# Optimization experiments

Hardware: AMD Instinct MI355X
Metric: run time of the kernel (lower is better)

The kernel has to match this reference:

```python
import jax, jax.numpy as jnp
import numpy as np

DIM = 1024
H = 16
D = DIM // H
B = 4
N = 1024
SUPPRESS = 0.1
SCALE = D ** -0.5


def setup_inputs() -> dict:
    key = jax.random.key(0)
    ks = jax.random.split(key, 16)
    s = 0.02
    inp = {
        "x": jax.random.normal(ks[0], (B, N, DIM), jnp.float32),
        "padding_mask": jax.random.randint(ks[1], (B, N), 0, 2).astype(bool),
        "alibi_bias": jax.random.normal(ks[2], (1, H, N, N), jnp.float32),
        "Wq": jax.random.normal(ks[3], (DIM, DIM), jnp.float32) * s,
        "bq": jnp.zeros((DIM,), jnp.float32),
        "Wk": jax.random.normal(ks[4], (DIM, DIM), jnp.float32) * s,
        "bk": jnp.zeros((DIM,), jnp.float32),
        "Wv": jax.random.normal(ks[5], (DIM, DIM), jnp.float32) * s,
        "bv": jnp.zeros((DIM,), jnp.float32),
        "WqC": jax.random.normal(ks[6], (D, D), jnp.float32) * s,
        "WAC": jax.random.normal(ks[7], (D, D), jnp.float32) * s,
        "bC": jax.random.normal(ks[8], (D,), jnp.float32) * s,
        "Wqg": jax.random.normal(ks[9], (D, D), jnp.float32) * s,
        "WAg": jax.random.normal(ks[10], (D, D), jnp.float32) * s,
        "bg": jax.random.normal(ks[11], (D,), jnp.float32) * s,
        "Wo": jax.random.normal(ks[12], (DIM, DIM), jnp.float32) * s,
        "bo": jnp.zeros((DIM,), jnp.float32),
    }
    return inp


def reference(x, padding_mask, alibi_bias, Wq, bq, Wk, bk, Wv, bv,
              WqC, WAC, bC, Wqg, WAg, bg, Wo, bo):
    Bx, Nx, C = x.shape
    # QKV projections -> [B, H, N, D]
    q = (x @ Wq.T + bq).reshape(Bx, Nx, H, D).transpose(0, 2, 1, 3)
    k = (x @ Wk.T + bk).reshape(Bx, Nx, H, D).transpose(0, 2, 1, 3)
    v = (x @ Wv.T + bv).reshape(Bx, Nx, H, D).transpose(0, 2, 1, 3)
    # scores [B, H, N, N] with alibi then key padding mask
    scores = jnp.einsum("bhnd,bhmd->bhnm", q * SCALE, k)
    scores = scores + alibi_bias  # alibi covers all H heads, broadcasts over B
    scores = jnp.where(padding_mask[:, None, None, :], -jnp.inf, scores)
    attn = jax.nn.softmax(scores.astype(jnp.float32), axis=-1).astype(q.dtype)
    A = jnp.einsum("bhnm,bhmd->bhnd", attn, v)
    # per-head gated linear fusion (W_* are D x D, shared across heads)
    C2 = jnp.einsum("bhnd,ed->bhne", q, WqC) + jnp.einsum("bhnd,ed->bhne", A, WAC) + bC
    g = jax.nn.sigmoid(jnp.einsum("bhnd,ed->bhne", q, Wqg) + jnp.einsum("bhnd,ed->bhne", A, WAg) + bg)
    G = (jnp.exp(g) + 1.0) * SUPPRESS
    Aega = G * C2  # [B, H, N, D]
    out = Aega.transpose(0, 2, 1, 3).reshape(Bx, Nx, C)
    return out @ Wo.T + bo
```

## Files before the change

### kernel.cpp

```cpp
#include <hip/hip_runtime.h>
#include <stdint.h>
#include <stddef.h>

#define SEQ   1024
#define CD    1024
#define NHD   16
#define HDD   64
#define NBB   4

typedef unsigned short u16t;
typedef __attribute__((ext_vector_type(4))) float f32x4;
typedef __attribute__((ext_vector_type(4))) unsigned int u32x4;
typedef __attribute__((ext_vector_type(8))) _Float16 f16x8;
typedef __attribute__((ext_vector_type(4))) unsigned short u16x4;

__device__ __forceinline__ u16t f2h(float f) {
  _Float16 h = (_Float16)f;
  return __builtin_bit_cast(u16t, h);
}

__device__ __forceinline__ f32x4 MFMA(u32x4 a, u32x4 b, f32x4 c) {
  return __builtin_amdgcn_mfma_f32_16x16x32_f16(
      __builtin_bit_cast(f16x8, a), __builtin_bit_cast(f16x8, b), c, 0, 0, 0);
}

struct ConvArgs {
  const float* src[9];
  u16t* dst[9];
  int n[9];
};

__global__ void conv_kernel(ConvArgs a) {
  const int tid = blockIdx.x * blockDim.x + threadIdx.x;
  const int nth = gridDim.x * blockDim.x;
  for (int s = 0; s < 9; ++s) {
    const float4* src = (const float4*)a.src[s];
    u16x4* dst = (u16x4*)a.dst[s];
    const int n4 = a.n[s] >> 2;
    for (int i = tid; i < n4; i += nth) {
      float4 f = src[i];
      u16x4 o = { f2h(f.x), f2h(f.y), f2h(f.z), f2h(f.w) };
      dst[i] = o;
    }
  }
}

__global__ void mask_prep_kernel(const void* __restrict__ mask,
                                 float* __restrict__ maskbias) {
  __shared__ int notI32, notU8;
  if (threadIdx.x == 0) { notI32 = 0; notU8 = 0; }
  __syncthreads();
  const unsigned int* mi = (const unsigned int*)mask;
  const unsigned char* mb = (const unsigned char*)mask;
  int nI = 0, nU = 0;
  for (int i = threadIdx.x; i < 1024; i += 256) {
    if (mi[i] > 1u) nI = 1;
  }
  for (int i = threadIdx.x; i < 4096; i += 256) {
    if (mb[i] > 1) nU = 1;
  }
  if (nI) atomicOr(&notI32, 1);
  if (nU) atomicOr(&notU8, 1);
  __syncthreads();
  const int mode = (!notI32) ? 0 : ((!notU8) ? 1 : 2);
  for (int i = threadIdx.x; i < NBB * SEQ; i += 256) {
    bool m;
    if (mode == 0)      m = mi[i] != 0u;
    else if (mode == 1) m = mb[i] != 0;
    else                m = ((const float*)mask)[i] != 0.0f;
    maskbias[i] = m ? -1e30f : 0.0f;
  }
}

template <int MODE>
__global__ __launch_bounds__(256, 2) void gemm_kernel(
    const u16t* __restrict__ A,
    const u16t* __restrict__ B0, const u16t* __restrict__ B1,
    const u16t* __restrict__ B2,
    const float* __restrict__ bias0, const float* __restrict__ bias1,
    const float* __restrict__ bias2,
    void* __restrict__ out0, void* __restrict__ out1, void* __restrict__ out2) {
  __shared__ alignas(16) u16t As[128][40];
  __shared__ alignas(16) u16t Bs[128][40];

  const int tid = threadIdx.x;
  const int m0 = blockIdx.x * 128;
  int n0, mat = 0;
  const u16t* Bsel;
  const float* biassel;
  if constexpr (MODE == 0) {
    mat = (int)blockIdx.y >> 3;
    n0 = ((int)blockIdx.y & 7) * 128;
    Bsel = (mat == 0) ? B0 : ((mat == 1) ? B1 : B2);
    biassel = (mat == 0) ? bias0 : ((mat == 1) ? bias1 : bias2);
  } else {
    n0 = (int)blockIdx.y * 128;
    Bsel = B0;
    biassel = bias0;
  }

  const int sr = tid >> 1;
  const int sc = (tid & 1) * 16;
  const int wid = tid >> 6, lane = tid & 63;
  const int l16 = lane & 15, lq = lane >> 4;
  const int wr = (wid >> 1) * 64, wc = (wid & 1) * 64;

  f32x4 acc[4][4] = {};

  const u16t* Aptr = A + (size_t)(m0 + sr) * CD + sc;
  const u16t* Bptr = Bsel + (size_t)(n0 + sr) * CD + sc;

  for (int k0 = 0; k0 < CD; k0 += 32) {
    u32x4 av0 = *(const u32x4*)(Aptr + k0);
    u32x4 av1 = *(const u32x4*)(Aptr + k0 + 8);
    u32x4 bv0 = *(const u32x4*)(Bptr + k0);
    u32x4 bv1 = *(const u32x4*)(Bptr + k0 + 8);
    __syncthreads();
    *(u32x4*)(&As[sr][sc]) = av0;
    *(u32x4*)(&As[sr][sc + 8]) = av1;
    *(u32x4*)(&Bs[sr][sc]) = bv0;
    *(u32x4*)(&Bs[sr][sc + 8]) = bv1;
    __syncthreads();
    u32x4 af[4], bf[4];
#pragma unroll
    for (int i = 0; i < 4; ++i) {
      af[i] = *(const u32x4*)(&As[wr + i * 16 + l16][lq * 8]);
      bf[i] = *(const u32x4*)(&Bs[wc + i * 16 + l16][lq * 8]);
    }
#pragma unroll
    for (int i = 0; i < 4; ++i)
#pragma unroll
      for (int j = 0; j < 4; ++j)
        acc[i][j] = MFMA(af[i], bf[j], acc[i][j]);
  }

  if constexpr (MODE == 1) {
    float* outp = (float*)out0;
#pragma unroll
    for (int i = 0; i < 4; ++i) {
#pragma unroll
      for (int j = 0; j < 4; ++j) {
        const int col = n0 + wc + j * 16 + l16;
        const float bb = biassel[col];
#pragma unroll
        for (int r = 0; r < 4; ++r) {
          const int row = m0 + wr + i * 16 + lq * 4 + r;
          outp[(size_t)row * CD + col] = acc[i][j][r] + bb;
        }
      }
    }
  } else {
    u16t* outp = (mat == 0) ? (u16t*)out0 : ((mat == 1) ? (u16t*)out1 : (u16t*)out2);
#pragma unroll
    for (int i = 0; i < 4; ++i) {
#pragma unroll
      for (int j = 0; j < 4; ++j) {
        const int cl = n0 + wc + j * 16 + l16;
        const int hh = cl >> 6, dd = cl & 63;
        const float bb = biassel[cl];
#pragma unroll
        for (int r = 0; r < 4; ++r) {
          const int row = m0 + wr + i * 16 + lq * 4 + r;
          const int bidx = row >> 10, nidx = row & 1023;
          outp[(((size_t)(bidx * NHD + hh)) * SEQ + nidx) * HDD + dd] =
              f2h(acc[i][j][r] + bb);
        }
      }
    }
  }
}

__global__ __launch_bounds__(256, 2) void attn_kernel(
    const u16t* __restrict__ Q, const u16t* __restrict__ K,
    const u16t* __restrict__ V, const float* __restrict__ alibi,
    const float* __restrict__ maskbias, u16t* __restrict__ Aout) {
  __shared__ alignas(16) u16t Ks[64][72];
  __shared__ alignas(16) u16t Vt[64][72];
  __shared__ alignas(16) u16t Ps[4][16][72];

  const int qt = blockIdx.x, h = blockIdx.y, b = blockIdx.z;
  const int tid = threadIdx.x, wid = tid >> 6, lane = tid & 63;
  const int l16 = lane & 15, lq = lane >> 4;
  const size_t hoff = ((size_t)(b * NHD + h)) * SEQ * HDD;
  const float* al = alibi + (size_t)h * SEQ * SEQ;
  const float* mb = maskbias + b * SEQ;
  const int q0 = qt * 64 + wid * 16;

  const u32x4 qf0 = *(const u32x4*)(Q + hoff + (size_t)(q0 + l16) * HDD + lq * 8);
  const u32x4 qf1 = *(const u32x4*)(Q + hoff + (size_t)(q0 + l16) * HDD + 32 + lq * 8);

  f32x4 Oacc[4] = {};
  float mrow[4] = {-1e30f, -1e30f, -1e30f, -1e30f};
  float lrow[4] = {0.f, 0.f, 0.f, 0.f};

  const int sr = tid >> 2;
  const int sc = (tid & 3) * 16;

  for (int k0 = 0; k0 < SEQ; k0 += 64) {
    u32x4 kv0 = *(const u32x4*)(K + hoff + (size_t)(k0 + sr) * HDD + sc);
    u32x4 kv1 = *(const u32x4*)(K + hoff + (size_t)(k0 + sr) * HDD + sc + 8);
    u32x4 vv0 = *(const u32x4*)(V + hoff + (size_t)(k0 + sr) * HDD + sc);
    u32x4 vv1 = *(const u32x4*)(V + hoff + (size_t)(k0 + sr) * HDD + sc + 8);
    __syncthreads();
    *(u32x4*)(&Ks[sr][sc]) = kv0;
    *(u32x4*)(&Ks[sr][sc + 8]) = kv1;
    {
      const u16t* pv = (const u16t*)&vv0;
#pragma unroll
      for (int e = 0; e < 8; ++e) Vt[sc + e][sr] = pv[e];
      pv = (const u16t*)&vv1;
#pragma unroll
      for (int e = 0; e < 8; ++e) Vt[sc + 8 + e][sr] = pv[e];
    }
    __syncthreads();

    f32x4 s[4];
#pragma unroll
    for (int kt = 0; kt < 4; ++kt) {
      u32x4 kf0 = *(const u32x4*)(&Ks[kt * 16 + l16][lq * 8]);
      u32x4 kf1 = *(const u32x4*)(&Ks[kt * 16 + l16][32 + lq * 8]);
      f32x4 z = {};
      z = MFMA(qf0, kf0, z);
      z = MFMA(qf1, kf1, z);
      s[kt] = z;
    }
#pragma unroll
    for (int kt = 0; kt < 4; ++kt) {
      const int kc = k0 + kt * 16 + l16;
      const float mbv = mb[kc];
#pragma unroll
      for (int r = 0; r < 4; ++r) {
        const int qr = q0 + lq * 4 + r;
        s[kt][r] = s[kt][r] * 0.125f + al[(size_t)qr * SEQ + kc] + mbv;
      }
    }
    float corr[4];
#pragma unroll
    for (int r = 0; r < 4; ++r) {
      float mx = fmaxf(fmaxf(s[0][r], s[1][r]), fmaxf(s[2][r], s[3][r]));
#pragma unroll
      for (int off = 1; off < 16; off <<= 1)
        mx = fmaxf(mx, __shfl_xor(mx, off, 64));
      const float mnew = fmaxf(mrow[r], mx);
      corr[r] = __expf(mrow[r] - mnew);
      mrow[r] = mnew;
      float ps = 0.f;
#pragma unroll
      for (int kt = 0; kt < 4; ++kt) {
        const float p = __expf(s[kt][r] - mnew);
        s[kt][r] = p;
        ps += p;
      }
#pragma unroll
      for (int off = 1; off < 16; off <<= 1)
        ps += __shfl_xor(ps, off, 64);
      lrow[r] = lrow[r] * corr[r] + ps;
    }
#pragma unroll
    for (int dt = 0; dt < 4; ++dt)
#pragma unroll
      for (int r = 0; r < 4; ++r)
        Oacc[dt][r] *= corr[r];

#pragma unroll
    for (int kt = 0; kt < 4; ++kt)
#pragma unroll
      for (int r = 0; r < 4; ++r)
        Ps[wid][lq * 4 + r][kt * 16 + l16] = f2h(s[kt][r]);

    const u32x4 pf0 = *(const u32x4*)(&Ps[wid][l16][lq * 8]);
    const u32x4 pf1 = *(const u32x4*)(&Ps[wid][l16][32 + lq * 8]);
#pragma unroll
    for (int dt = 0; dt < 4; ++dt) {
      u32x4 vf0 = *(const u32x4*)(&Vt[dt * 16 + l16][lq * 8]);
      u32x4 vf1 = *(const u32x4*)(&Vt[dt * 16 + l16][32 + lq * 8]);
      Oacc[dt] = MFMA(pf0, vf0, Oacc[dt]);
      Oacc[dt] = MFMA(pf1, vf1, Oacc[dt]);
    }
  }

#pragma unroll
  for (int r = 0; r < 4; ++r) {
    const float inv = 1.0f / lrow[r];
    const int qr = q0 + lq * 4 + r;
#pragma unroll
    for (int dt = 0; dt < 4; ++dt)
      Aout[hoff + (size_t)qr * HDD + dt * 16 + l16] = f2h(Oacc[dt][r] * inv);
  }
}

__global__ __launch_bounds__(256, 2) void fuse_kernel(
    const u16t* __restrict__ Q, const u16t* __restrict__ Aatt,
    const u16t* __restrict__ W4, const float* __restrict__ bC,
    const float* __restrict__ bg, u16t* __restrict__ Aega) {
  __shared__ alignas(16) u16t Ws[4][64][72];
  const int tid = threadIdx.x;
  for (int i = tid; i < 2048; i += 256) {
    const int w = i >> 9;
    const int r = (i >> 3) & 63;
    const int c = (i & 7) * 8;
    *(u32x4*)(&Ws[w][r][c]) = *(const u32x4*)(W4 + (size_t)(w * 64 + r) * 64 + c);
  }
  __syncthreads();
  const int wid = tid >> 6, lane = tid & 63;
  const int l16 = lane & 15, lq = lane >> 4;
  const size_t row0 = (size_t)blockIdx.x * 64 + wid * 16;

  const u32x4 qf0 = *(const u32x4*)(Q + (row0 + l16) * HDD + lq * 8);
  const u32x4 qf1 = *(const u32x4*)(Q + (row0 + l16) * HDD + 32 + lq * 8);
  const u32x4 af0 = *(const u32x4*)(Aatt + (row0 + l16) * HDD + lq * 8);
  const u32x4 af1 = *(const u32x4*)(Aatt + (row0 + l16) * HDD + 32 + lq * 8);

#pragma unroll
  for (int et = 0; et < 4; ++et) {
    u32x4 wc0 = *(const u32x4*)(&Ws[0][et * 16 + l16][lq * 8]);
    u32x4 wc1 = *(const u32x4*)(&Ws[0][et * 16 + l16][32 + lq * 8]);
    u32x4 wa0 = *(const u32x4*)(&Ws[1][et * 16 + l16][lq * 8]);
    u32x4 wa1 = *(const u32x4*)(&Ws[1][et * 16 + l16][32 + lq * 8]);
    u32x4 wg0 = *(const u32x4*)(&Ws[2][et * 16 + l16][lq * 8]);
    u32x4 wg1 = *(const u32x4*)(&Ws[2][et * 16 + l16][32 + lq * 8]);
    u32x4 wh0 = *(const u32x4*)(&Ws[3][et * 16 + l16][lq * 8]);
    u32x4 wh1 = *(const u32x4*)(&Ws[3][et * 16 + l16][32 + lq * 8]);
    f32x4 c2 = {};
    c2 = MFMA(qf0, wc0, c2);
    c2 = MFMA(qf1, wc1, c2);
    c2 = MFMA(af0, wa0, c2);
    c2 = MFMA(af1, wa1, c2);
    f32x4 gg = {};
    gg = MFMA(qf0, wg0, gg);
    gg = MFMA(qf1, wg1, gg);
    gg = MFMA(af0, wh0, gg);
    gg = MFMA(af1, wh1, gg);
    const int e = et * 16 + l16;
    const float bCe = bC[e], bge = bg[e];
#pragma unroll
    for (int r = 0; r < 4; ++r) {
      const size_t row = row0 + lq * 4 + r;
      const int bidx = (int)(row >> 14);
      const int hh = (int)((row >> 10) & 15);
      const int nn = (int)(row & 1023);
      const float C2v = c2[r] + bCe;
      const float gv = 1.f / (1.f + __expf(-(gg[r] + bge)));
      const float Gv = (__expf(gv) + 1.f) * 0.1f;
      Aega[((size_t)(bidx * SEQ + nn)) * CD + hh * 64 + e] = f2h(Gv * C2v);
    }
  }
}

static constexpr size_t OFF_X16 = 0;
static constexpr size_t OFF_WQ  = 8388608;
static constexpr size_t OFF_WK  = 10485760;
static constexpr size_t OFF_WV  = 12582912;
static constexpr size_t OFF_WO  = 14680064;
static constexpr size_t OFF_W4  = 16777216;
static constexpr size_t OFF_MB  = 16809984;
static constexpr size_t OFF_Q   = 16826368;
static constexpr size_t OFF_K   = 25214976;
static constexpr size_t OFF_V   = 33603584;
static constexpr size_t OFF_A   = 41992192;
static constexpr size_t OFF_AEG = 50380800;

extern "C" void kernel_launch(void* const* d_in, const int* in_sizes, int n_in,
                              void* d_out, int out_size, void* d_ws, size_t ws_size,
                              hipStream_t stream) {
  const float* x     = (const float*)d_in[0];
  const void*  pmask = d_in[1];
  const float* alibi = (const float*)d_in[2];
  const float* Wq    = (const float*)d_in[3];
  const float* bq    = (const float*)d_in[4];
  const float* Wk    = (const float*)d_in[5];
  const float* bk    = (const float*)d_in[6];
  const float* Wv    = (const float*)d_in[7];
  const float* bv    = (const float*)d_in[8];
  const float* WqC   = (const float*)d_in[9];
  const float* WAC   = (const float*)d_in[10];
  const float* bC    = (const float*)d_in[11];
  const float* Wqg   = (const float*)d_in[12];
  const float* WAg   = (const float*)d_in[13];
  const float* bg    = (const float*)d_in[14];
  const float* Wo    = (const float*)d_in[15];
  const float* bo    = (const float*)d_in[16];

  char* w = (char*)d_ws;
  u16t* X16 = (u16t*)(w + OFF_X16);
  u16t* WQp = (u16t*)(w + OFF_WQ);
  u16t* WKp = (u16t*)(w + OFF_WK);
  u16t* WVp = (u16t*)(w + OFF_WV);
  u16t* WOp = (u16t*)(w + OFF_WO);
  u16t* W4p = (u16t*)(w + OFF_W4);
  float* MBp = (float*)(w + OFF_MB);
  u16t* Qb  = (u16t*)(w + OFF_Q);
  u16t* Kb  = (u16t*)(w + OFF_K);
  u16t* Vb  = (u16t*)(w + OFF_V);
  u16t* Ab  = (u16t*)(w + OFF_A);
  u16t* AEG = (u16t*)(w + OFF_AEG);

  ConvArgs ca;
  ca.src[0] = x;   ca.dst[0] = X16;            ca.n[0] = 4 * 1024 * 1024;
  ca.src[1] = Wq;  ca.dst[1] = WQp;            ca.n[1] = 1024 * 1024;
  ca.src[2] = Wk;  ca.dst[2] = WKp;            ca.n[2] = 1024 * 1024;
  ca.src[3] = Wv;  ca.dst[3] = WVp;            ca.n[3] = 1024 * 1024;
  ca.src[4] = Wo;  ca.dst[4] = WOp;            ca.n[4] = 1024 * 1024;
  ca.src[5] = WqC; ca.dst[5] = W4p;            ca.n[5] = 4096;
  ca.src[6] = WAC; ca.dst[6] = W4p + 4096;     ca.n[6] = 4096;
  ca.src[7] = Wqg; ca.dst[7] = W4p + 8192;     ca.n[7] = 4096;
  ca.src[8] = WAg; ca.dst[8] = W4p + 12288;    ca.n[8] = 4096;

  hipLaunchKernelGGL(conv_kernel, dim3(1024), dim3(256), 0, stream, ca);
  hipLaunchKernelGGL(mask_prep_kernel, dim3(1), dim3(256), 0, stream, pmask, MBp);
  hipLaunchKernelGGL(HIP_KERNEL_NAME(gemm_kernel<0>), dim3(32, 24), dim3(256), 0,
                     stream, X16, WQp, WKp, WVp, bq, bk, bv,
                     (void*)Qb, (void*)Kb, (void*)Vb);
  hipLaunchKernelGGL(attn_kernel, dim3(16, 16, 4), dim3(256), 0, stream,
                     Qb, Kb, Vb, alibi, MBp, Ab);
  hipLaunchKernelGGL(fuse_kernel, dim3(1024), dim3(256), 0, stream,
                     Qb, Ab, W4p, bC, bg, AEG);
  hipLaunchKernelGGL(HIP_KERNEL_NAME(gemm_kernel<1>), dim3(32, 8), dim3(256), 0,
                     stream, AEG, WOp, (const u16t*)nullptr, (const u16t*)nullptr,
                     bo, (const float*)nullptr, (const float*)nullptr,
                     d_out, (void*)nullptr, (void*)nullptr);
}
```

Baseline: 162.5 us.

## Use direct global-to-LDS loads in GEMM, pre-transposed V and pipelined attention

The GEMM now stages A/B tiles with global_load_lds instead of register round-trips and drops the padded LDS layout. The QKV GEMM writes V already transposed, so attention no longer scatters V into LDS element by element. Attention computes S transposed, so each lane holds one query row and softmax needs fewer shuffles. P is passed to the PV MFMA through register shuffles instead of LDS, and K/V/alibi loads are software-prefetched one tile ahead with occupancy raised to 3. Losing the LDS padding may introduce bank conflicts, and the strided transposed V store is less coalesced.

```diff
diff --git a/kernel.cpp b/kernel.cpp
--- a/kernel.cpp
+++ b/kernel.cpp
@@ -22,6 +22,12 @@
 __device__ __forceinline__ f32x4 MFMA(u32x4 a, u32x4 b, f32x4 c) {
   return __builtin_amdgcn_mfma_f32_16x16x32_f16(
       __builtin_bit_cast(f16x8, a), __builtin_bit_cast(f16x8, b), c, 0, 0, 0);
+}
+
+__device__ __forceinline__ void gl_lds16(const u16t* g, u16t* l) {
+  __builtin_amdgcn_global_load_lds(
+      (const __attribute__((address_space(1))) unsigned int*)g,
+      (__attribute__((address_space(3))) unsigned int*)l, 16, 0, 0);
 }
 
 struct ConvArgs {
@@ -80,8 +86,8 @@
     const float* __restrict__ bias0, const float* __restrict__ bias1,
     const float* __restrict__ bias2,
     void* __restrict__ out0, void* __restrict__ out1, void* __restrict__ out2) {
-  __shared__ alignas(16) u16t As[128][40];
-  __shared__ alignas(16) u16t Bs[128][40];
+  __shared__ alignas(16) u16t As[128 * 32];
+  __shared__ alignas(16) u16t Bs[128 * 32];
 
   const int tid = threadIdx.x;
   const int m0 = blockIdx.x * 128;
@@ -99,33 +105,31 @@
     biassel = bias0;
   }
 
-  const int sr = tid >> 1;
-  const int sc = (tid & 1) * 16;
   const int wid = tid >> 6, lane = tid & 63;
   const int l16 = lane & 15, lq = lane >> 4;
   const int wr = (wid >> 1) * 64, wc = (wid & 1) * 64;
 
+  const int srow = lane >> 2;
+  const int scol = (lane & 3) * 8;
+  const u16t* Ag = A + (size_t)(m0 + wid * 32 + srow) * CD + scol;
+  const u16t* Bg = Bsel + (size_t)(n0 + wid * 32 + srow) * CD + scol;
+  u16t* AsW = &As[(wid * 32 + srow) * 32 + scol];
+  u16t* BsW = &Bs[(wid * 32 + srow) * 32 + scol];
+
   f32x4 acc[4][4] = {};
 
-  const u16t* Aptr = A + (size_t)(m0 + sr) * CD + sc;
-  const u16t* Bptr = Bsel + (size_t)(n0 + sr) * CD + sc;
-
   for (int k0 = 0; k0 < CD; k0 += 32) {
-    u32x4 av0 = *(const u32x4*)(Aptr + k0);
-    u32x4 av1 = *(const u32x4*)(Aptr + k0 + 8);
-    u32x4 bv0 = *(const u32x4*)(Bptr + k0);
-    u32x4 bv1 = *(const u32x4*)(Bptr + k0 + 8);
     __syncthreads();
-    *(u32x4*)(&As[sr][sc]) = av0;
-    *(u32x4*)(&As[sr][sc + 8]) = av1;
-    *(u32x4*)(&Bs[sr][sc]) = bv0;
-    *(u32x4*)(&Bs[sr][sc + 8]) = bv1;
+    gl_lds16(Ag + k0, AsW);
+    gl_lds16(Ag + k0 + (size_t)16 * CD, AsW + 16 * 32);
+    gl_lds16(Bg + k0, BsW);
+    gl_lds16(Bg + k0 + (size_t)16 * CD, BsW + 16 * 32);
     __syncthreads();
     u32x4 af[4], bf[4];
 #pragma unroll
     for (int i = 0; i < 4; ++i) {
-      af[i] = *(const u32x4*)(&As[wr + i * 16 + l16][lq * 8]);
-      bf[i] = *(const u32x4*)(&Bs[wc + i * 16 + l16][lq * 8]);
+      af[i] = *(const u32x4*)(&As[(wr + i * 16 + l16) * 32 + lq * 8]);
+      bf[i] = *(const u32x4*)(&Bs[(wc + i * 16 + l16) * 32 + lq * 8]);
     }
 #pragma unroll
     for (int i = 0; i < 4; ++i)
@@ -162,57 +166,82 @@
         for (int r = 0; r < 4; ++r) {
           const int row = m0 + wr + i * 16 + lq * 4 + r;
           const int bidx = row >> 10, nidx = row & 1023;
-          outp[(((size_t)(bidx * NHD + hh)) * SEQ + nidx) * HDD + dd] =
-              f2h(acc[i][j][r] + bb);
+          if (mat == 2) {
+            outp[(((size_t)(bidx * NHD + hh)) * HDD + dd) * SEQ + nidx] =
+                f2h(acc[i][j][r] + bb);
+          } else {
+            outp[(((size_t)(bidx * NHD + hh)) * SEQ + nidx) * HDD + dd] =
+                f2h(acc[i][j][r] + bb);
+          }
         }
       }
     }
   }
 }
 
-__global__ __launch_bounds__(256, 2) void attn_kernel(
+__global__ __launch_bounds__(256, 3) void attn_kernel(
     const u16t* __restrict__ Q, const u16t* __restrict__ K,
-    const u16t* __restrict__ V, const float* __restrict__ alibi,
+    const u16t* __restrict__ VT, const float* __restrict__ alibi,
     const float* __restrict__ maskbias, u16t* __restrict__ Aout) {
   __shared__ alignas(16) u16t Ks[64][72];
-  __shared__ alignas(16) u16t Vt[64][72];
-  __shared__ alignas(16) u16t Ps[4][16][72];
+  __shared__ alignas(16) u16t Vts[64][72];
 
   const int qt = blockIdx.x, h = blockIdx.y, b = blockIdx.z;
   const int tid = threadIdx.x, wid = tid >> 6, lane = tid & 63;
   const int l16 = lane & 15, lq = lane >> 4;
   const size_t hoff = ((size_t)(b * NHD + h)) * SEQ * HDD;
-  const float* al = alibi + (size_t)h * SEQ * SEQ;
+  const int q0 = qt * 64 + wid * 16;
+  const float* al = alibi + (size_t)h * SEQ * SEQ + (size_t)(q0 + l16) * SEQ;
   const float* mb = maskbias + b * SEQ;
-  const int q0 = qt * 64 + wid * 16;
 
   const u32x4 qf0 = *(const u32x4*)(Q + hoff + (size_t)(q0 + l16) * HDD + lq * 8);
   const u32x4 qf1 = *(const u32x4*)(Q + hoff + (size_t)(q0 + l16) * HDD + 32 + lq * 8);
 
   f32x4 Oacc[4] = {};
-  float mrow[4] = {-1e30f, -1e30f, -1e30f, -1e30f};
-  float lrow[4] = {0.f, 0.f, 0.f, 0.f};
+  float mrow = -1e30f, lrow = 0.f;
 
   const int sr = tid >> 2;
   const int sc = (tid & 3) * 16;
-
-  for (int k0 = 0; k0 < SEQ; k0 += 64) {
-    u32x4 kv0 = *(const u32x4*)(K + hoff + (size_t)(k0 + sr) * HDD + sc);
-    u32x4 kv1 = *(const u32x4*)(K + hoff + (size_t)(k0 + sr) * HDD + sc + 8);
-    u32x4 vv0 = *(const u32x4*)(V + hoff + (size_t)(k0 + sr) * HDD + sc);
-    u32x4 vv1 = *(const u32x4*)(V + hoff + (size_t)(k0 + sr) * HDD + sc + 8);
-    __syncthreads();
+  const u16t* Kg = K + hoff + (size_t)sr * HDD + sc;
+  const u16t* Vg = VT + hoff + (size_t)sr * SEQ + sc;
+
+  u32x4 kv0 = *(const u32x4*)(Kg);
+  u32x4 kv1 = *(const u32x4*)(Kg + 8);
+  u32x4 vv0 = *(const u32x4*)(Vg);
+  u32x4 vv1 = *(const u32x4*)(Vg + 8);
+  f32x4 ali[2][4];
+#pragma unroll
+  for (int kt = 0; kt < 4; ++kt)
+    ali[0][kt] = *(const f32x4*)(al + kt * 16 + lq * 4);
+
+#pragma unroll 2
+  for (int t = 0; t < 16; ++t) {
+    const int k0 = t * 64;
+    const int tc = t & 1, tn = (t + 1) & 1;
+    asm volatile("" ::: "memory");
+    __builtin_amdgcn_s_barrier();
+    asm volatile("" ::: "memory");
     *(u32x4*)(&Ks[sr][sc]) = kv0;
     *(u32x4*)(&Ks[sr][sc + 8]) = kv1;
+    *(u32x4*)(&Vts[sr][sc]) = vv0;
+    *(u32x4*)(&Vts[sr][sc + 8]) = vv1;
     {
-      const u16t* pv = (const u16t*)&vv0;
-#pragma unroll
-      for (int e = 0; e < 8; ++e) Vt[sc + e][sr] = pv[e];
-      pv = (const u16t*)&vv1;
-#pragma unroll
-      for (int e = 0; e < 8; ++e) Vt[sc + 8 + e][sr] = pv[e];
-    }
-    __syncthreads();
+      const int kn = (t < 15) ? (k0 + 64) : 0;
+      kv0 = *(const u32x4*)(Kg + (size_t)kn * HDD);
+      kv1 = *(const u32x4*)(Kg + (size_t)kn * HDD + 8);
+      vv0 = *(const u32x4*)(Vg + kn);
+      vv1 = *(const u32x4*)(Vg + kn + 8);
+    }
+    asm volatile("s_waitcnt lgkmcnt(0)" ::: "memory");
+    __builtin_amdgcn_s_barrier();
+    asm volatile("" ::: "memory");
+
+    {
+      const float* aln = al + ((t < 15) ? (k0 + 64) : 0);
+#pragma unroll
+      for (int kt = 0; kt < 4; ++kt)
+        ali[tn][kt] = *(const f32x4*)(aln + kt * 16 + lq * 4);
+    }
 
     f32x4 s[4];
 #pragma unroll
@@ -220,72 +249,76 @@
       u32x4 kf0 = *(const u32x4*)(&Ks[kt * 16 + l16][lq * 8]);
       u32x4 kf1 = *(const u32x4*)(&Ks[kt * 16 + l16][32 + lq * 8]);
       f32x4 z = {};
-      z = MFMA(qf0, kf0, z);
-      z = MFMA(qf1, kf1, z);
+      z = MFMA(kf0, qf0, z);
+      z = MFMA(kf1, qf1, z);
       s[kt] = z;
     }
 #pragma unroll
     for (int kt = 0; kt < 4; ++kt) {
-      const int kc = k0 + kt * 16 + l16;
-      const float mbv = mb[kc];
+      const f32x4 a4 = ali[tc][kt];
+      const f32x4 m4 = *(const f32x4*)(mb + k0 + kt * 16 + lq * 4);
+#pragma unroll
+      for (int r = 0; r < 4; ++r)
+        s[kt][r] = s[kt][r] * 0.125f + a4[r] + m4[r];
+    }
+    float mx = s[0][0];
+#pragma unroll
+    for (int kt = 0; kt < 4; ++kt)
+#pragma unroll
+      for (int r = 0; r < 4; ++r) mx = fmaxf(mx, s[kt][r]);
+    mx = fmaxf(mx, __shfl_xor(mx, 16, 64));
+    mx = fmaxf(mx, __shfl_xor(mx, 32, 64));
+    const float mnew = fmaxf(mrow, mx);
+    const float corr = __expf(mrow - mnew);
+    mrow = mnew;
+    float ps = 0.f;
+#pragma unroll
+    for (int kt = 0; kt < 4; ++kt)
 #pragma unroll
       for (int r = 0; r < 4; ++r) {
-        const int qr = q0 + lq * 4 + r;
-        s[kt][r] = s[kt][r] * 0.125f + al[(size_t)qr * SEQ + kc] + mbv;
-      }
-    }
-    float corr[4];
-#pragma unroll
-    for (int r = 0; r < 4; ++r) {
-      float mx = fmaxf(fmaxf(s[0][r], s[1][r]), fmaxf(s[2][r], s[3][r]));
-#pragma unroll
-      for (int off = 1; off < 16; off <<= 1)
-        mx = fmaxf(mx, __shfl_xor(mx, off, 64));
-      const float mnew = fmaxf(mrow[r], mx);
-      corr[r] = __expf(mrow[r] - mnew);
-      mrow[r] = mnew;
-      float ps = 0.f;
-#pragma unroll
-      for (int kt = 0; kt < 4; ++kt) {
         const float p = __expf(s[kt][r] - mnew);
         s[kt][r] = p;
         ps += p;
       }
-#pragma unroll
-      for (int off = 1; off < 16; off <<= 1)
-        ps += __shfl_xor(ps, off, 64);
-      lrow[r] = lrow[r] * corr[r] + ps;
-    }
+    ps += __shfl_xor(ps, 16, 64);
+    ps += __shfl_xor(ps, 32, 64);
+    lrow = lrow * corr + ps;
+#pragma unroll
+    for (int r = 0; r < 4; ++r) {
+      const float cr = __shfl(corr, lq * 4 + r, 64);
+      Oacc[0][r] *= cr; Oacc[1][r] *= cr; Oacc[2][r] *= cr; Oacc[3][r] *= cr;
+    }
+    unsigned int wp[4][2];
+#pragma unroll
+    for (int kt = 0; kt < 4; ++kt) {
+      wp[kt][0] = (unsigned)f2h(s[kt][0]) | ((unsigned)f2h(s[kt][1]) << 16);
+      wp[kt][1] = (unsigned)f2h(s[kt][2]) | ((unsigned)f2h(s[kt][3]) << 16);
+    }
+#pragma unroll
+    for (int ks = 0; ks < 2; ++ks) {
+      u32x4 pa;
+#pragma unroll
+      for (int m = 0; m < 4; ++m) {
+        const int srcl = l16 + ((lq & 1) << 5) + ((m >> 1) << 4);
+        const unsigned lo = __shfl(wp[ks * 2][m & 1], srcl, 64);
+        const unsigned hi = __shfl(wp[ks * 2 + 1][m & 1], srcl, 64);
+        pa[m] = (lq & 2) ? hi : lo;
+      }
+#pragma unroll
+      for (int dt = 0; dt < 4; ++dt) {
+        u32x4 vf = *(const u32x4*)(&Vts[dt * 16 + l16][ks * 32 + lq * 8]);
+        Oacc[dt] = MFMA(pa, vf, Oacc[dt]);
+      }
+    }
+  }
+
+#pragma unroll
+  for (int r = 0; r < 4; ++r) {
+    const float linv = 1.0f / __shfl(lrow, lq * 4 + r, 64);
+    const int qr = q0 + lq * 4 + r;
 #pragma unroll
     for (int dt = 0; dt < 4; ++dt)
-#pragma unroll
-      for (int r = 0; r < 4; ++r)
-        Oacc[dt][r] *= corr[r];
-
-#pragma unroll
-    for (int kt = 0; kt < 4; ++kt)
-#pragma unroll
-      for (int r = 0; r < 4; ++r)
-        Ps[wid][lq * 4 + r][kt * 16 + l16] = f2h(s[kt][r]);
-
-    const u32x4 pf0 = *(const u32x4*)(&Ps[wid][l16][lq * 8]);
-    const u32x4 pf1 = *(const u32x4*)(&Ps[wid][l16][32 + lq * 8]);
-#pragma unroll
-    for (int dt = 0; dt < 4; ++dt) {
-      u32x4 vf0 = *(const u32x4*)(&Vt[dt * 16 + l16][lq * 8]);
-      u32x4 vf1 = *(const u32x4*)(&Vt[dt * 16 + l16][32 + lq * 8]);
-      Oacc[dt] = MFMA(pf0, vf0, Oacc[dt]);
-      Oacc[dt] = MFMA(pf1, vf1, Oacc[dt]);
-    }
-  }
-
-#pragma unroll
-  for (int r = 0; r < 4; ++r) {
-    const float inv = 1.0f / lrow[r];
-    const int qr = q0 + lq * 4 + r;
-#pragma unroll
-    for (int dt = 0; dt < 4; ++dt)
-      Aout[hoff + (size_t)qr * HDD + dt * 16 + l16] = f2h(Oacc[dt][r] * inv);
+      Aout[hoff + (size_t)qr * HDD + dt * 16 + l16] = f2h(Oacc[dt][r] * linv);
   }
 }
 
@@ -391,7 +424,7 @@
   float* MBp = (float*)(w + OFF_MB);
   u16t* Qb  = (u16t*)(w + OFF_Q);
   u16t* Kb  = (u16t*)(w + OFF_K);
-  u16t* Vb  = (u16t*)(w + OFF_V);
+  u16t* VTb = (u16t*)(w + OFF_V);
   u16t* Ab  = (u16t*)(w + OFF_A);
   u16t* AEG = (u16t*)(w + OFF_AEG);
 
@@ -410,9 +443,9 @@
   hipLaunchKernelGGL(mask_prep_kernel, dim3(1), dim3(256), 0, stream, pmask, MBp);
   hipLaunchKernelGGL(HIP_KERNEL_NAME(gemm_kernel<0>), dim3(32, 24), dim3(256), 0,
                      stream, X16, WQp, WKp, WVp, bq, bk, bv,
-                     (void*)Qb, (void*)Kb, (void*)Vb);
+                     (void*)Qb, (void*)Kb, (void*)VTb);
   hipLaunchKernelGGL(attn_kernel, dim3(16, 16, 4), dim3(256), 0, stream,
-                     Qb, Kb, Vb, alibi, MBp, Ab);
+                     Qb, Kb, VTb, alibi, MBp, Ab);
   hipLaunchKernelGGL(fuse_kernel, dim3(1024), dim3(256), 0, stream,
                      Qb, Ab, W4p, bC, bg, AEG);
   hipLaunchKernelGGL(HIP_KERNEL_NAME(gemm_kernel<1>), dim3(32, 8), dim3(256), 0,
```

Result: no change. 162.4 us (-0.1%).
